# Performance work log

Hardware: AMD Instinct MI355X
Metric: run time of the kernel (lower is better)

The kernel has to match this reference:

```python
import jax, jax.numpy as jnp
import numpy as np

N, D = 8192, 512
LN_EPS = 1e-5


def setup_inputs() -> dict:
    key = jax.random.key(0)
    ks = jax.random.split(key, 7)
    s = 1.0 / np.sqrt(D)
    return {
        "image_features": jax.random.normal(ks[0], (N, D), dtype=jnp.float32),
        "Wq": jax.random.normal(ks[1], (D, D), dtype=jnp.float32) * s,
        "bq": jax.random.normal(ks[2], (D,), dtype=jnp.float32) * s,
        "Wk": jax.random.normal(ks[3], (D, D), dtype=jnp.float32) * s,
        "bk": jax.random.normal(ks[4], (D,), dtype=jnp.float32) * s,
        "Wv": jax.random.normal(ks[5], (D, D), dtype=jnp.float32) * s,
        "bv": jax.random.normal(ks[6], (D,), dtype=jnp.float32) * s,
        "gamma": jnp.ones((D,), dtype=jnp.float32),
        "beta": jnp.zeros((D,), dtype=jnp.float32),
    }


def reference(image_features, Wq, bq, Wk, bk, Wv, bv, gamma, beta):
    x = image_features                      # [N, D]
    q = x @ Wq.T + bq                       # [N, D]
    k = x @ Wk.T + bk                       # [N, D]
    v = x @ Wv.T + bv                       # [N, D]
    # Unscaled single-head attention: softmax over dim 1 (keys)
    scores = q @ k.T                        # [N, N]
    attn = jax.nn.softmax(scores, axis=1)   # [N, N]
    attn_out = attn @ v                     # [N, D]
    # Residual + LayerNorm over last dim
    h = x + attn_out
    mu = jnp.mean(h, axis=-1, keepdims=True)
    var = jnp.mean(jnp.square(h - mu), axis=-1, keepdims=True)
    residual = (h - mu) * jax.lax.rsqrt(var + LN_EPS) * gamma + beta
    # Mean pool over the N regions, keepdim -> [1, D]
    return jnp.mean(residual, axis=0, keepdims=True)
```

## Files before the change

kernel.cpp:

```cpp
#include <hip/hip_runtime.h>
#include <stdint.h>


#define NR 8192
#define DI 512

typedef float f32x4 __attribute__((ext_vector_type(4)));
typedef short short8 __attribute__((ext_vector_type(8)));
typedef unsigned short u16;

__device__ __forceinline__ u16 f2bf(float f) {
  union { float f; unsigned u; } v; v.f = f;
  unsigned u = v.u;
  return (u16)((u + 0x7FFFu + ((u >> 16) & 1u)) >> 16);
}
__device__ __forceinline__ float bf2f(u16 b) {
  union { unsigned u; float f; } v; v.u = ((unsigned)b) << 16;
  return v.f;
}

__device__ __forceinline__ void load_lds16(const void* g, void* l) {
  __builtin_amdgcn_global_load_lds(
      (const __attribute__((address_space(1))) unsigned int*)g,
      (__attribute__((address_space(3))) unsigned int*)l, 16, 0, 0);
}

__global__ void k_prep(const float* __restrict__ x,
                       const float* __restrict__ wq,
                       const float* __restrict__ wk,
                       const float* __restrict__ wv,
                       u16* __restrict__ xhi, u16* __restrict__ whi) {
  int tid = blockIdx.x * 256 + threadIdx.x;
  int nth = gridDim.x * 256;
  const float4* x4 = (const float4*)x;
  ushort4* xh4 = (ushort4*)xhi;
  for (int i = tid; i < NR * DI / 4; i += nth) {
    float4 v = x4[i];
    ushort4 h;
    h.x = f2bf(v.x); h.y = f2bf(v.y); h.z = f2bf(v.z); h.w = f2bf(v.w);
    xh4[i] = h;
  }
  ushort4* wh4 = (ushort4*)whi;
  const int wq4 = DI * DI / 4;
  for (int i = tid; i < 3 * wq4; i += nth) {
    int z = i / wq4, j = i - z * wq4;
    const float4* src = (const float4*)(z == 0 ? wq : z == 1 ? wk : wv);
    float4 v = src[j];
    ushort4 h;
    h.x = f2bf(v.x); h.y = f2bf(v.y); h.z = f2bf(v.z); h.w = f2bf(v.w);
    wh4[i] = h;
  }
}

__global__ __launch_bounds__(256, 4) void k_qkv(
    const u16* __restrict__ xhi, const u16* __restrict__ whi,
    const float* __restrict__ bq, const float* __restrict__ bk,
    const float* __restrict__ bv,
    u16* __restrict__ qhi, u16* __restrict__ khi,
    u16* __restrict__ vt, float* __restrict__ qnp) {
  __shared__ __align__(16) u16 sA[128 * 64], sB[128 * 64];
  const int z = blockIdx.z;
  const int m0 = blockIdx.y * 128, n0 = blockIdx.x * 128;
  const int lane = threadIdx.x & 63, wid = threadIdx.x >> 6;
  const int wr = wid >> 1, wc = wid & 1;
  const u16* Wh = whi + (size_t)z * DI * DI;
  f32x4 acc[4][4] = {};
  const bool isA = wid < 2;
  const u16* gS = isA ? xhi : Wh;
  u16* Dst = isA ? sA : sB;
  const int gb = isA ? m0 : n0;
  const int rbase = (wid & 1) * 64;

  for (int kt = 0; kt < 8; ++kt) {
#pragma unroll
    for (int c = 0; c < 8; ++c) {
      int row = rbase + c * 8 + (lane >> 3);
      int srck = kt * 64 + (((lane & 7) ^ (row & 7)) << 3);
      load_lds16(gS + (size_t)(gb + row) * DI + srck,
                 (char*)Dst + (size_t)(rbase + c * 8) * 128);
    }
    __syncthreads();
#pragma unroll
    for (int dt = 0; dt < 2; ++dt) {
      short8 a[4], b[4];
      int kb = dt * 64 + ((lane >> 4) << 4);
#pragma unroll
      for (int t = 0; t < 4; ++t) {
        int ra = wr * 64 + t * 16 + (lane & 15);
        a[t] = *(const short8*)((const char*)sA + ra * 128 + (kb ^ ((ra & 7) << 4)));
        int rb = wc * 64 + t * 16 + (lane & 15);
        b[t] = *(const short8*)((const char*)sB + rb * 128 + (kb ^ ((rb & 7) << 4)));
      }
#pragma unroll
      for (int mi = 0; mi < 4; ++mi)
#pragma unroll
        for (int ni = 0; ni < 4; ++ni)
          acc[mi][ni] = __builtin_amdgcn_mfma_f32_16x16x32_bf16(a[mi], b[ni], acc[mi][ni], 0, 0, 0);
    }
    __syncthreads();
  }

  const float* bias = (z == 0) ? bq : (z == 1) ? bk : bv;
  if (z < 2) {
    u16* oh = (z == 0) ? qhi : khi;
    float rowsq[4][4] = {};
#pragma unroll
    for (int ni = 0; ni < 4; ++ni) {
      int col = n0 + wc * 64 + ni * 16 + (lane & 15);
      float b = bias[col];
#pragma unroll
      for (int mi = 0; mi < 4; ++mi)
#pragma unroll
        for (int r = 0; r < 4; ++r) {
          int row = m0 + wr * 64 + mi * 16 + (lane >> 4) * 4 + r;
          float v = acc[mi][ni][r] + b;
          oh[(size_t)row * DI + col] = f2bf(v);
          if (z == 0) rowsq[mi][r] += v * v;
        }
    }
    if (z == 0) {
#pragma unroll
      for (int mi = 0; mi < 4; ++mi)
#pragma unroll
        for (int r = 0; r < 4; ++r) {
          float s = rowsq[mi][r];
          s += __shfl_xor(s, 1); s += __shfl_xor(s, 2);
          s += __shfl_xor(s, 4); s += __shfl_xor(s, 8);
          if ((lane & 15) == 0) {
            int row = m0 + wr * 64 + mi * 16 + (lane >> 4) * 4 + r;
            qnp[(size_t)(blockIdx.x * 2 + wc) * NR + row] = s;
          }
        }
    }
  } else {
#pragma unroll
    for (int ni = 0; ni < 4; ++ni) {
      int col = n0 + wc * 64 + ni * 16 + (lane & 15);
      float b = bias[col];
#pragma unroll
      for (int mi = 0; mi < 4; ++mi) {
        int rowb = m0 + wr * 64 + mi * 16 + (lane >> 4) * 4;
        ushort4 pk;
        pk.x = f2bf(acc[mi][ni][0] + b);
        pk.y = f2bf(acc[mi][ni][1] + b);
        pk.z = f2bf(acc[mi][ni][2] + b);
        pk.w = f2bf(acc[mi][ni][3] + b);
        *(ushort4*)(vt + (size_t)col * NR + rowb) = pk;
      }
    }
  }
}

__global__ void k_cvec(const float* __restrict__ qnp, float* __restrict__ cvec) {
  int i = blockIdx.x * 256 + threadIdx.x;
  float s = 0.f;
#pragma unroll
  for (int t = 0; t < 8; ++t) s += qnp[(size_t)t * NR + i];
  cvec[i] = 5.0f * sqrtf(s) + 10.f;
}

__global__ __launch_bounds__(256, 4) void k_scores(
    const u16* __restrict__ qhi, const u16* __restrict__ khi,
    const float* __restrict__ cvec,
    u16* __restrict__ P, float* __restrict__ psum) {
  __shared__ __align__(16) u16 sA[128 * 64], sB[128 * 64];
  const int m0 = blockIdx.y * 128, n0 = blockIdx.x * 128;
  const int lane = threadIdx.x & 63, wid = threadIdx.x >> 6;
  const int wr = wid >> 1, wc = wid & 1;
  f32x4 acc[4][4] = {};
  const bool isA = wid < 2;
  const u16* gS = isA ? qhi : khi;
  u16* Dst = isA ? sA : sB;
  const int gb = isA ? m0 : n0;
  const int rbase = (wid & 1) * 64;

  for (int kt = 0; kt < 8; ++kt) {
#pragma unroll
    for (int c = 0; c < 8; ++c) {
      int row = rbase + c * 8 + (lane >> 3);
      int srck = kt * 64 + (((lane & 7) ^ (row & 7)) << 3);
      load_lds16(gS + (size_t)(gb + row) * DI + srck,
                 (char*)Dst + (size_t)(rbase + c * 8) * 128);
    }
    __syncthreads();
#pragma unroll
    for (int dt = 0; dt < 2; ++dt) {
      short8 a[4], b[4];
      int kb = dt * 64 + ((lane >> 4) << 4);
#pragma unroll
      for (int t = 0; t < 4; ++t) {
        int ra = wr * 64 + t * 16 + (lane & 15);
        a[t] = *(const short8*)((const char*)sA + ra * 128 + (kb ^ ((ra & 7) << 4)));
        int rb = wc * 64 + t * 16 + (lane & 15);
        b[t] = *(const short8*)((const char*)sB + rb * 128 + (kb ^ ((rb & 7) << 4)));
      }
#pragma unroll
      for (int mi = 0; mi < 4; ++mi)
#pragma unroll
        for (int ni = 0; ni < 4; ++ni)
          acc[mi][ni] = __builtin_amdgcn_mfma_f32_16x16x32_bf16(a[mi], b[ni], acc[mi][ni], 0, 0, 0);
    }
    __syncthreads();
  }

  float cr[4][4];
#pragma unroll
  for (int mi = 0; mi < 4; ++mi)
#pragma unroll
    for (int r = 0; r < 4; ++r)
      cr[mi][r] = cvec[m0 + wr * 64 + mi * 16 + (lane >> 4) * 4 + r];

  float ps[4][4] = {};
#pragma unroll
  for (int ni = 0; ni < 4; ++ni) {
    int col = n0 + wc * 64 + ni * 16 + (lane & 15);
#pragma unroll
    for (int mi = 0; mi < 4; ++mi)
#pragma unroll
      for (int r = 0; r < 4; ++r) {
        int row = m0 + wr * 64 + mi * 16 + (lane >> 4) * 4 + r;
        float a = fminf(acc[mi][ni][r] - cr[mi][r], 60.f);
        float p = __expf(a);
        P[(size_t)row * NR + col] = f2bf(p);
        ps[mi][r] += p;
      }
  }
#pragma unroll
  for (int mi = 0; mi < 4; ++mi)
#pragma unroll
    for (int r = 0; r < 4; ++r) {
      float s = ps[mi][r];
      s += __shfl_xor(s, 1); s += __shfl_xor(s, 2);
      s += __shfl_xor(s, 4); s += __shfl_xor(s, 8);
      if ((lane & 15) == 0) {
        int row = m0 + wr * 64 + mi * 16 + (lane >> 4) * 4 + r;
        psum[(size_t)(blockIdx.x * 2 + wc) * NR + row] = s;
      }
    }
}

__global__ void k_rowsum(const float* __restrict__ psum, float* __restrict__ rinv) {
  int i = blockIdx.x * 256 + threadIdx.x;
  float s = 0.f;
  for (int t = 0; t < 128; ++t) s += psum[(size_t)t * NR + i];
  rinv[i] = (s > 0.f) ? 1.f / s : 0.f;
}

__global__ __launch_bounds__(256, 4) void k_pv(
    const u16* __restrict__ P, const u16* __restrict__ vt,
    u16* __restrict__ Opart) {
  __shared__ __align__(16) u16 sA[128 * 64], sB[128 * 64];
  const int m0 = blockIdx.y * 128, n0 = blockIdx.x * 128;
  const int z = blockIdx.z;
  const int lane = threadIdx.x & 63;
  const int wid = threadIdx.x >> 6;
  const int wr = wid >> 1, wc = wid & 1;

  f32x4 acc[4][4] = {};
  const bool isA = wid < 2;
  const u16* gS = isA ? P : vt;
  u16* Dst = isA ? sA : sB;
  const int gb = isA ? m0 : n0;
  const int rbase = (wid & 1) * 64;

  for (int kt = 0; kt < 64; ++kt) {
    int kg = z * 4096 + kt * 64;
#pragma unroll
    for (int c = 0; c < 8; ++c) {
      int row = rbase + c * 8 + (lane >> 3);
      int srck = kg + (((lane & 7) ^ (row & 7)) << 3);
      load_lds16(gS + (size_t)(gb + row) * NR + srck,
                 (char*)Dst + (size_t)(rbase + c * 8) * 128);
    }
    __syncthreads();
#pragma unroll
    for (int dt = 0; dt < 2; ++dt) {
      short8 a[4], b[4];
      int kb = dt * 64 + ((lane >> 4) << 4);
#pragma unroll
      for (int t = 0; t < 4; ++t) {
        int ra = wr * 64 + t * 16 + (lane & 15);
        a[t] = *(const short8*)((const char*)sA + ra * 128 + (kb ^ ((ra & 7) << 4)));
        int rb = wc * 64 + t * 16 + (lane & 15);
        b[t] = *(const short8*)((const char*)sB + rb * 128 + (kb ^ ((rb & 7) << 4)));
      }
#pragma unroll
      for (int mi = 0; mi < 4; ++mi)
#pragma unroll
        for (int ni = 0; ni < 4; ++ni)
          acc[mi][ni] = __builtin_amdgcn_mfma_f32_16x16x32_bf16(a[mi], b[ni], acc[mi][ni], 0, 0, 0);
    }
    __syncthreads();
  }
#pragma unroll
  for (int ni = 0; ni < 4; ++ni) {
    int col = n0 + wc * 64 + ni * 16 + (lane & 15);
#pragma unroll
    for (int mi = 0; mi < 4; ++mi)
#pragma unroll
      for (int r = 0; r < 4; ++r) {
        int row = m0 + wr * 64 + mi * 16 + (lane >> 4) * 4 + r;
        Opart[((size_t)z * NR + row) * DI + col] = f2bf(acc[mi][ni][r]);
      }
  }
}

__global__ __launch_bounds__(256) void k_ln(const u16* __restrict__ Opart,
                                            const float* __restrict__ x,
                                            const float* __restrict__ rinv,
                                            const float* __restrict__ gamma,
                                            const float* __restrict__ beta,
                                            float* __restrict__ part) {
  const int lane = threadIdx.x & 63;
  const int w = threadIdx.x >> 6;
  float4 g0 = *(const float4*)(gamma + lane * 8);
  float4 g1 = *(const float4*)(gamma + lane * 8 + 4);
  float4 b0 = *(const float4*)(beta + lane * 8);
  float4 b1 = *(const float4*)(beta + lane * 8 + 4);
  float ga[8] = {g0.x, g0.y, g0.z, g0.w, g1.x, g1.y, g1.z, g1.w};
  float be[8] = {b0.x, b0.y, b0.z, b0.w, b1.x, b1.y, b1.z, b1.w};
  float colacc[8] = {0, 0, 0, 0, 0, 0, 0, 0};
  for (int it = 0; it < 32; ++it) {
    int row = blockIdx.x * 128 + it * 4 + w;
    float rv = rinv[row];
    const u16* o0r = Opart + (size_t)row * DI + lane * 8;
    const u16* o1r = o0r + (size_t)NR * DI;
    const float* xr = x + (size_t)row * DI + lane * 8;
    short8 s0 = *(const short8*)o0r;
    short8 s1 = *(const short8*)o1r;
    float4 xa = *(const float4*)xr;
    float4 xb = *(const float4*)(xr + 4);
    float xv[8] = {xa.x, xa.y, xa.z, xa.w, xb.x, xb.y, xb.z, xb.w};
    float v[8];
#pragma unroll
    for (int j = 0; j < 8; ++j)
      v[j] = (bf2f((u16)s0[j]) + bf2f((u16)s1[j])) * rv + xv[j];
    float s1s = 0.f, s2s = 0.f;
#pragma unroll
    for (int j = 0; j < 8; ++j) { s1s += v[j]; s2s += v[j] * v[j]; }
#pragma unroll
    for (int m = 1; m < 64; m <<= 1) { s1s += __shfl_xor(s1s, m); s2s += __shfl_xor(s2s, m); }
    float mean = s1s * (1.f / DI);
    float var = fmaxf(s2s * (1.f / DI) - mean * mean, 0.f);
    float rstd = rsqrtf(var + 1e-5f);
#pragma unroll
    for (int j = 0; j < 8; ++j) colacc[j] += (v[j] - mean) * rstd * ga[j] + be[j];
  }
  __shared__ float red[4][DI];
#pragma unroll
  for (int j = 0; j < 8; ++j) red[w][lane * 8 + j] = colacc[j];
  __syncthreads();
  for (int d = threadIdx.x; d < DI; d += 256)
    part[(size_t)blockIdx.x * DI + d] = red[0][d] + red[1][d] + red[2][d] + red[3][d];
}

__global__ void k_final(const float* __restrict__ part, float* __restrict__ out) {
  int d = threadIdx.x;
  float s = 0.f;
  for (int t = 0; t < 64; ++t) s += part[(size_t)t * DI + d];
  out[d] = s * (1.f / NR);
}

extern "C" void kernel_launch(void* const* d_in, const int* in_sizes, int n_in,
                              void* d_out, int out_size, void* d_ws, size_t ws_size,
                              hipStream_t stream) {
  (void)in_sizes; (void)n_in; (void)out_size; (void)ws_size;
  const float* x = (const float*)d_in[0];
  const float* wq = (const float*)d_in[1];
  const float* bq = (const float*)d_in[2];
  const float* wk = (const float*)d_in[3];
  const float* bk = (const float*)d_in[4];
  const float* wv = (const float*)d_in[5];
  const float* bv = (const float*)d_in[6];
  const float* gamma = (const float*)d_in[7];
  const float* beta = (const float*)d_in[8];
  float* out = (float*)d_out;

  char* cur = (char*)d_ws;
  auto alloc = [&](size_t bytes) -> char* {
    char* p = cur;
    cur += (bytes + 255) & ~(size_t)255;
    return p;
  };
  u16* xhi = (u16*)alloc((size_t)NR * DI * 2);
  u16* whi = (u16*)alloc((size_t)3 * DI * DI * 2);
  u16* qhi = (u16*)alloc((size_t)NR * DI * 2);
  u16* khi = (u16*)alloc((size_t)NR * DI * 2);
  u16* vt = (u16*)alloc((size_t)DI * NR * 2);
  float* qnp = (float*)alloc((size_t)8 * NR * 4);
  float* cvec = (float*)alloc((size_t)NR * 4);
  float* psum = (float*)alloc((size_t)128 * NR * 4);
  float* rinv = (float*)alloc((size_t)NR * 4);
  u16* P = (u16*)alloc((size_t)NR * NR * 2);
  u16* Opart = (u16*)alloc((size_t)2 * NR * DI * 2);
  float* part = (float*)alloc((size_t)64 * DI * 4);

  k_prep<<<1024, 256, 0, stream>>>(x, wq, wk, wv, xhi, whi);
  k_qkv<<<dim3(4, 64, 3), 256, 0, stream>>>(xhi, whi, bq, bk, bv,
                                            qhi, khi, vt, qnp);
  k_cvec<<<32, 256, 0, stream>>>(qnp, cvec);
  k_scores<<<dim3(64, 64), 256, 0, stream>>>(qhi, khi, cvec, P, psum);
  k_rowsum<<<32, 256, 0, stream>>>(psum, rinv);
  k_pv<<<dim3(4, 64, 2), 256, 0, stream>>>(P, vt, Opart);
  k_ln<<<64, 256, 0, stream>>>(Opart, x, rinv, gamma, beta, part);
  k_final<<<1, 512, 0, stream>>>(part, out);
}
```

Measured before the change: 237.7 us.

## Skip negligible softmax tiles in PV GEMM using per-tile activity bitmasks

The row-sum kernel now also builds, for each 16-row group, a bitmask of which 64-column key tiles hold normalized probability mass above 1e-7. The PV kernel reads these masks and skips both the global-to-LDS loads of P and the MFMAs for inactive row-group/tile pairs. V tiles are still loaded every step. Because the attention is unscaled and the softmax is very peaked, most tiles should be skippable. The cost is a small bounded approximation error and extra psum reads in the row-sum kernel.

```diff
diff --git a/kernel.cpp b/kernel.cpp
--- a/kernel.cpp
+++ b/kernel.cpp
@@ -4,10 +4,12 @@
 
 #define NR 8192
 #define DI 512
+#define ACT_THR 1e-7f
 
 typedef float f32x4 __attribute__((ext_vector_type(4)));
 typedef short short8 __attribute__((ext_vector_type(8)));
 typedef unsigned short u16;
+typedef unsigned long long u64;
 
 __device__ __forceinline__ u16 f2bf(float f) {
   union { float f; unsigned u; } v; v.f = f;
@@ -239,15 +241,33 @@
     }
 }
 
-__global__ void k_rowsum(const float* __restrict__ psum, float* __restrict__ rinv) {
+__global__ void k_rowsum(const float* __restrict__ psum,
+                         float* __restrict__ rinv,
+                         u64* __restrict__ actbits) {
   int i = blockIdx.x * 256 + threadIdx.x;
   float s = 0.f;
   for (int t = 0; t < 128; ++t) s += psum[(size_t)t * NR + i];
-  rinv[i] = (s > 0.f) ? 1.f / s : 0.f;
+  float inv = (s > 0.f) ? 1.f / s : 0.f;
+  rinv[i] = inv;
+  u64 b0 = 0, b1 = 0;
+  for (int t = 0; t < 64; ++t)
+    if (psum[(size_t)t * NR + i] * inv > ACT_THR) b0 |= (1ull << t);
+  for (int t = 0; t < 64; ++t)
+    if (psum[(size_t)(t + 64) * NR + i] * inv > ACT_THR) b1 |= (1ull << t);
+#pragma unroll
+  for (int d = 1; d < 16; d <<= 1) {
+    b0 |= __shfl_xor(b0, d);
+    b1 |= __shfl_xor(b1, d);
+  }
+  if ((threadIdx.x & 15) == 0) {
+    actbits[(size_t)(i >> 4) * 2 + 0] = b0;
+    actbits[(size_t)(i >> 4) * 2 + 1] = b1;
+  }
 }
 
 __global__ __launch_bounds__(256, 4) void k_pv(
     const u16* __restrict__ P, const u16* __restrict__ vt,
+    const u64* __restrict__ actbits,
     u16* __restrict__ Opart) {
   __shared__ __align__(16) u16 sA[128 * 64], sB[128 * 64];
   const int m0 = blockIdx.y * 128, n0 = blockIdx.x * 128;
@@ -263,14 +283,30 @@
   const int gb = isA ? m0 : n0;
   const int rbase = (wid & 1) * 64;
 
+  u64 actg[8];
+#pragma unroll
+  for (int j = 0; j < 8; ++j)
+    actg[j] = actbits[(size_t)((m0 >> 4) + j) * 2 + z];
+
   for (int kt = 0; kt < 64; ++kt) {
     int kg = z * 4096 + kt * 64;
-#pragma unroll
-    for (int c = 0; c < 8; ++c) {
-      int row = rbase + c * 8 + (lane >> 3);
-      int srck = kg + (((lane & 7) ^ (row & 7)) << 3);
-      load_lds16(gS + (size_t)(gb + row) * NR + srck,
-                 (char*)Dst + (size_t)(rbase + c * 8) * 128);
+    if (isA) {
+#pragma unroll
+      for (int c = 0; c < 8; ++c) {
+        if (!((actg[(rbase >> 4) + (c >> 1)] >> kt) & 1)) continue;
+        int row = rbase + c * 8 + (lane >> 3);
+        int srck = kg + (((lane & 7) ^ (row & 7)) << 3);
+        load_lds16(gS + (size_t)(gb + row) * NR + srck,
+                   (char*)Dst + (size_t)(rbase + c * 8) * 128);
+      }
+    } else {
+#pragma unroll
+      for (int c = 0; c < 8; ++c) {
+        int row = rbase + c * 8 + (lane >> 3);
+        int srck = kg + (((lane & 7) ^ (row & 7)) << 3);
+        load_lds16(gS + (size_t)(gb + row) * NR + srck,
+                   (char*)Dst + (size_t)(rbase + c * 8) * 128);
+      }
     }
     __syncthreads();
 #pragma unroll
@@ -279,16 +315,18 @@
       int kb = dt * 64 + ((lane >> 4) << 4);
 #pragma unroll
       for (int t = 0; t < 4; ++t) {
-        int ra = wr * 64 + t * 16 + (lane & 15);
-        a[t] = *(const short8*)((const char*)sA + ra * 128 + (kb ^ ((ra & 7) << 4)));
         int rb = wc * 64 + t * 16 + (lane & 15);
         b[t] = *(const short8*)((const char*)sB + rb * 128 + (kb ^ ((rb & 7) << 4)));
       }
 #pragma unroll
-      for (int mi = 0; mi < 4; ++mi)
+      for (int mi = 0; mi < 4; ++mi) {
+        if (!((actg[wr * 4 + mi] >> kt) & 1)) continue;
+        int ra = wr * 64 + mi * 16 + (lane & 15);
+        a[mi] = *(const short8*)((const char*)sA + ra * 128 + (kb ^ ((ra & 7) << 4)));
 #pragma unroll
         for (int ni = 0; ni < 4; ++ni)
           acc[mi][ni] = __builtin_amdgcn_mfma_f32_16x16x32_bf16(a[mi], b[ni], acc[mi][ni], 0, 0, 0);
+      }
     }
     __syncthreads();
   }
@@ -391,6 +429,7 @@
   float* cvec = (float*)alloc((size_t)NR * 4);
   float* psum = (float*)alloc((size_t)128 * NR * 4);
   float* rinv = (float*)alloc((size_t)NR * 4);
+  u64* actbits = (u64*)alloc((size_t)512 * 2 * 8);
   u16* P = (u16*)alloc((size_t)NR * NR * 2);
   u16* Opart = (u16*)alloc((size_t)2 * NR * DI * 2);
   float* part = (float*)alloc((size_t)64 * DI * 4);
@@ -400,8 +439,8 @@
                                             qhi, khi, vt, qnp);
   k_cvec<<<32, 256, 0, stream>>>(qnp, cvec);
   k_scores<<<dim3(64, 64), 256, 0, stream>>>(qhi, khi, cvec, P, psum);
-  k_rowsum<<<32, 256, 0, stream>>>(psum, rinv);
-  k_pv<<<dim3(4, 64, 2), 256, 0, stream>>>(P, vt, Opart);
+  k_rowsum<<<32, 256, 0, stream>>>(psum, rinv, actbits);
+  k_pv<<<dim3(4, 64, 2), 256, 0, stream>>>(P, vt, actbits, Opart);
   k_ln<<<64, 256, 0, stream>>>(Opart, x, rinv, gamma, beta, part);
   k_final<<<1, 512, 0, stream>>>(part, out);
 }
```

After: 362.4 us. 52.5% more time.
